# Optimization experiments

Hardware: AMD Instinct MI355X
Metric: run time of the kernel (lower is better)

## Reference

```python
import jax, jax.numpy as jnp
import numpy as np

PI = jnp.pi

def phasor_encode(x):
    # map phase in [-1,1] to unit complex phasor exp(i*pi*x)
    return jnp.exp(jnp.complex64(1j) * PI * x.astype(jnp.float32))

def phasor_act(z):
    # angle of complex activation, normalized back to [-1,1]
    return jnp.angle(z) / PI

def multi_dense(x, w, b):
    # PhasorMultiDense: x [b,t,d], w [h,d,D], b [h,D] (complex bias, ones init)
    xz = phasor_encode(x)                                      # [b,t,d] complex64
    wz = w.astype(jnp.complex64)
    bz = b.astype(jnp.complex64)
    yz = jnp.einsum('btd,hdD->bhtD', xz, wz) + bz[None, :, None, :]
    return phasor_act(yz)                                      # [b,h,t,D] real

def attend(q, k, v):
    # VSA phasor attention: similarity = Re(qz . conj(kz)) / d, softmax, complex bundle of v phasors
    d = q.shape[-1]
    qz = phasor_encode(q)
    kz = phasor_encode(k)
    scores = jnp.real(jnp.einsum('bhtd,bhTd->bhtT', qz, jnp.conj(kz))) / d
    probs = jax.nn.softmax(scores, axis=-1)
    vz = phasor_encode(v)
    out = jnp.einsum('bhtT,bhTd->bhtd', probs.astype(jnp.complex64), vz)
    return phasor_act(out)                                     # [b,h,t,D]

def setup_inputs() -> dict:
    key = jax.random.key(0)
    ks = jax.random.split(key, 8)
    B, Tq, Tkv, D, H = 2, 1024, 1024, 512, 8
    sw = 1.0 / np.sqrt(D)       # VarianceScaling(1.0) fan_in
    swo = 1.0 / np.sqrt(H * D)
    return {
        'query': jax.random.uniform(ks[0], (B, Tq, D), jnp.float32, -1.0, 1.0),
        'keyvalue': jax.random.uniform(ks[1], (B, Tkv, D), jnp.float32, -1.0, 1.0),
        'wq': jax.random.normal(ks[2], (H, D, D), jnp.float32) * sw,
        'bq': jnp.ones((H, D), jnp.float32),
        'wk': jax.random.normal(ks[3], (H, D, D), jnp.float32) * sw,
        'bk': jnp.ones((H, D), jnp.float32),
        'wv': jax.random.normal(ks[4], (H, D, D), jnp.float32) * sw,
        'bv': jnp.ones((H, D), jnp.float32),
        'wo': jax.random.normal(ks[5], (H * D, D), jnp.float32) * swo,
        'bo': jnp.ones((D,), jnp.float32),
    }

def reference(query, keyvalue, wq, bq, wk, bk, wv, bv, wo, bo):
    q = multi_dense(query, wq, bq)        # [b,h,t,D]
    k = multi_dense(keyvalue, wk, bk)
    v = multi_dense(keyvalue, wv, bv)
    r = attend(q, k, v)                   # [b,h,t,D]
    b_, h_, t_, d_ = r.shape
    r_flat = jnp.transpose(r, (0, 2, 1, 3)).reshape(b_, t_, h_ * d_)  # b t (h d)
    # final PhasorDense
    xz = phasor_encode(r_flat)
    z = jnp.einsum('btd,dD->btD', xz, wo.astype(jnp.complex64)) + bo.astype(jnp.complex64)
    return phasor_act(z)                  # [b, t_q, output_channels]
```

## Files before the change

kernel.cpp:

```cpp
#include <hip/hip_runtime.h>
#include <math.h>


#define PI_F 3.14159274101257324f

typedef __attribute__((ext_vector_type(8))) _Float16 half8;
typedef __attribute__((ext_vector_type(4))) _Float16 half4;
typedef __attribute__((ext_vector_type(2))) _Float16 half2v;
typedef __attribute__((ext_vector_type(4))) float f32x4;
typedef unsigned int u32;

#define MFMA16(a, b, c) __builtin_amdgcn_mfma_f32_16x16x32_f16((a), (b), (c), 0, 0, 0)

__device__ __forceinline__ void gll16(const void* g, void* l) {
    __builtin_amdgcn_global_load_lds(
        (const __attribute__((address_space(1))) u32*)g,
        (__attribute__((address_space(3))) u32*)l, 16, 0, 0);
}

#define MKSRC(U, NT, gh, gl, stride, sp, dp, dbase)                         \
    _Pragma("unroll") for (int u_ = 0; u_ < (U); ++u_) {                    \
        const int idx_ = u_ * (NT) + tid;                                   \
        const int row_ = idx_ >> 3, ss_ = idx_ & 7;                         \
        const int sl_ = ss_ ^ (row_ & 7);                                   \
        sp[u_] = ((sl_ < 4) ? (gh) : (gl)) + (size_t)row_ * (stride)        \
                 + (sl_ & 3) * 8;                                           \
        dp[u_] = (dbase) + idx_ * 16;                                       \
    }
#define STAGE(U, sp, dp, bufoff, kk)                                        \
    _Pragma("unroll") for (int u_ = 0; u_ < (U); ++u_)                      \
        gll16(sp[u_] + (kk), lds + (bufoff) + dp[u_]);

__device__ __forceinline__ half8 fragP(const char* ldsp, int row, int oct, int hilo) {
    const int sl = (oct + hilo * 4) ^ (row & 7);
    return *(const half8*)(ldsp + row * 128 + (sl << 4));
}

__device__ __forceinline__ void split2(float x, _Float16& h, _Float16& l) {
    _Float16 hh = (_Float16)x;
    h = hh;
    l = (_Float16)((x - (float)hh) * 4096.0f);
}

__global__ __launch_bounds__(256) void encode_phasor(
    const float* __restrict__ x,
    _Float16* __restrict__ ch, _Float16* __restrict__ cl,
    _Float16* __restrict__ sh, _Float16* __restrict__ sl)
{
    const int idx = blockIdx.x * 256 + threadIdx.x;
    float4 v = ((const float4*)x)[idx];
    float cc[4], ss[4];
    sincosf(PI_F * v.x, &ss[0], &cc[0]);
    sincosf(PI_F * v.y, &ss[1], &cc[1]);
    sincosf(PI_F * v.z, &ss[2], &cc[2]);
    sincosf(PI_F * v.w, &ss[3], &cc[3]);
    half4 chv, clv, shv, slv;
#pragma unroll
    for (int q = 0; q < 4; ++q) {
        _Float16 a, b;
        split2(cc[q], a, b); chv[q] = a; clv[q] = b;
        split2(ss[q], a, b); shv[q] = a; slv[q] = b;
    }
    ((half4*)ch)[idx] = chv;
    ((half4*)cl)[idx] = clv;
    ((half4*)sh)[idx] = shv;
    ((half4*)sl)[idx] = slv;
}

__global__ __launch_bounds__(256) void tsplit64(
    const float* __restrict__ w, _Float16* __restrict__ th, _Float16* __restrict__ tl,
    int K, int N)
{
    const int kt = blockIdx.x, ntile = blockIdx.y, h = blockIdx.z;
    const int k0 = kt * 64, n0 = ntile * 64;
    __shared__ float T[64][65];
    const int tid = threadIdx.x;
    const float* wb = w + (size_t)h * K * N;
    {
        const int r = tid >> 4, c4 = (tid & 15) * 4;
#pragma unroll
        for (int rr = 0; rr < 64; rr += 16) {
            float4 v = *(const float4*)&wb[(size_t)(k0 + rr + r) * N + n0 + c4];
            T[rr + r][c4 + 0] = v.x; T[rr + r][c4 + 1] = v.y;
            T[rr + r][c4 + 2] = v.z; T[rr + r][c4 + 3] = v.w;
        }
    }
    __syncthreads();
    {
        const int n = tid >> 2, kq = (tid & 3) * 16;
        half8 hv[2], lv[2];
#pragma unroll
        for (int q = 0; q < 16; ++q) {
            float f = T[kq + q][n];
            _Float16 hh, ll; split2(f, hh, ll);
            hv[q >> 3][q & 7] = hh; lv[q >> 3][q & 7] = ll;
        }
        _Float16* oh = th + ((size_t)h * N + n0 + n) * K + k0 + kq;
        _Float16* ol = tl + ((size_t)h * N + n0 + n) * K + k0 + kq;
        *(half8*)oh = hv[0]; *(half8*)(oh + 8) = hv[1];
        *(half8*)ol = lv[0]; *(half8*)(ol + 8) = lv[1];
    }
}

template<bool VT>
__global__ __launch_bounds__(256, 3) void proj_mfma(
    const _Float16* __restrict__ xch, const _Float16* __restrict__ xcl,
    const _Float16* __restrict__ xsh, const _Float16* __restrict__ xsl,
    const _Float16* __restrict__ wth, const _Float16* __restrict__ wtl,
    const float* __restrict__ bias,
    _Float16* __restrict__ o0h, _Float16* __restrict__ o0l,
    _Float16* __restrict__ vch, _Float16* __restrict__ vcl,
    _Float16* __restrict__ vsh, _Float16* __restrict__ vsl,
    int h0, int hcnt)
{
    const int m0 = blockIdx.x * 64;
    const int hc = blockIdx.y >> 3;
    const int n0 = (blockIdx.y & 7) * 64;
    __shared__ char lds[49152];
    const int tid = threadIdx.x, wv = tid >> 6, ln = tid & 63;
    const int wr = wv >> 1, wc = wv & 1, lm = ln & 15, oct = ln >> 4;

    const _Float16* sp_xc[2]; int dp_xc[2];
    const _Float16* sp_xs[2]; int dp_xs[2];
    const _Float16* sp_w[2];  int dp_w[2];
    MKSRC(2, 256, xch + (size_t)m0 * 512, xcl + (size_t)m0 * 512, 512, sp_xc, dp_xc, 0);
    MKSRC(2, 256, xsh + (size_t)m0 * 512, xsl + (size_t)m0 * 512, 512, sp_xs, dp_xs, 8192);
    const _Float16* wbh = wth + ((size_t)hc * 512 + n0) * 512;
    const _Float16* wbl = wtl + ((size_t)hc * 512 + n0) * 512;
    MKSRC(2, 256, wbh, wbl, 512, sp_w, dp_w, 16384);

    f32x4 ach[2][2] = {}, acl[2][2] = {}, ash[2][2] = {}, asl[2][2] = {};

    STAGE(2, sp_xc, dp_xc, 0, 0);
    STAGE(2, sp_xs, dp_xs, 0, 0);
    STAGE(2, sp_w,  dp_w,  0, 0);
    int off = 0;
    for (int s = 0; s < 16; ++s) {
        __syncthreads();
        const int nxt = off ^ 24576;
        if (s + 1 < 16) {
            const int kk = (s + 1) * 32;
            STAGE(2, sp_xc, dp_xc, nxt, kk);
            STAGE(2, sp_xs, dp_xs, nxt, kk);
            STAGE(2, sp_w,  dp_w,  nxt, kk);
        }
        const char* Xc = lds + off;
        const char* Xs = lds + off + 8192;
        const char* W  = lds + off + 16384;
        __builtin_amdgcn_s_setprio(1);
        half8 wh[2], wl[2];
#pragma unroll
        for (int j = 0; j < 2; ++j) {
            wh[j] = fragP(W, wc * 32 + j * 16 + lm, oct, 0);
            wl[j] = fragP(W, wc * 32 + j * 16 + lm, oct, 1);
        }
#pragma unroll
        for (int i = 0; i < 2; ++i) {
            const int ar = wr * 32 + i * 16 + lm;
            half8 c1 = fragP(Xc, ar, oct, 0);
            half8 c2 = fragP(Xc, ar, oct, 1);
            half8 s1 = fragP(Xs, ar, oct, 0);
            half8 s2 = fragP(Xs, ar, oct, 1);
#pragma unroll
            for (int j = 0; j < 2; ++j) {
                ach[i][j] = MFMA16(c1, wh[j], ach[i][j]);
                acl[i][j] = MFMA16(c1, wl[j], acl[i][j]);
                acl[i][j] = MFMA16(c2, wh[j], acl[i][j]);
                ash[i][j] = MFMA16(s1, wh[j], ash[i][j]);
                asl[i][j] = MFMA16(s1, wl[j], asl[i][j]);
                asl[i][j] = MFMA16(s2, wh[j], asl[i][j]);
            }
        }
        __builtin_amdgcn_s_setprio(0);
        off = nxt;
    }

    const float LS = 1.0f / 4096.0f;
    const int b = m0 >> 10, tbase = m0 & 1023;
    const size_t zz = (size_t)(b * hcnt + hc);
    if constexpr (!VT) {
#pragma unroll
        for (int j = 0; j < 2; ++j) {
            const int nloc = wc * 32 + j * 16 + lm;
            const float bval = bias[(size_t)(h0 + hc) * 512 + n0 + nloc];
#pragma unroll
            for (int i = 0; i < 2; ++i)
#pragma unroll
                for (int r = 0; r < 4; ++r) {
                    const int mloc = wr * 32 + i * 16 + oct * 4 + r;
                    float yc = ach[i][j][r] + acl[i][j][r] * LS + bval;
                    float ys = ash[i][j][r] + asl[i][j][r] * LS;
                    float inv = 1.0f / sqrtf(fmaxf(yc * yc + ys * ys, 1e-36f));
                    float c = yc * inv, sn = ys * inv;
                    _Float16 chh, chl, shh, shl;
                    split2(c, chh, chl); split2(sn, shh, shl);
                    const size_t offo = (zz * 1024 + tbase + mloc) * 1024 + 2 * (n0 + nloc);
                    half2v hv, lv;
                    hv[0] = chh; hv[1] = shh; lv[0] = chl; lv[1] = shl;
                    *(half2v*)(o0h + offo) = hv;
                    *(half2v*)(o0l + offo) = lv;
                }
        }
    } else {
#pragma unroll
        for (int q = 0; q < 2; ++q) {
            __syncthreads();
            if (wc == q) {
#pragma unroll
                for (int j = 0; j < 2; ++j) {
                    const int nloc = wc * 32 + j * 16 + lm;
                    const int dch = j * 16 + lm;
                    const float bval = bias[(size_t)(h0 + hc) * 512 + n0 + nloc];
#pragma unroll
                    for (int i = 0; i < 2; ++i)
#pragma unroll
                        for (int r = 0; r < 4; ++r) {
                            const int tloc = wr * 32 + i * 16 + oct * 4 + r;
                            float yc = ach[i][j][r] + acl[i][j][r] * LS + bval;
                            float ys = ash[i][j][r] + asl[i][j][r] * LS;
                            float inv = 1.0f / sqrtf(fmaxf(yc * yc + ys * ys, 1e-36f));
                            float c = yc * inv, sn = ys * inv;
                            _Float16 chh, chl, shh, shl;
                            split2(c, chh, chl); split2(sn, shh, shl);
                            ((_Float16*)(lds +     0))[dch * 68 + tloc] = chh;
                            ((_Float16*)(lds +  4352))[dch * 68 + tloc] = chl;
                            ((_Float16*)(lds +  8704))[dch * 68 + tloc] = shh;
                            ((_Float16*)(lds + 13056))[dch * 68 + tloc] = shl;
                        }
                }
            }
            __syncthreads();
            {
                const int p = tid >> 6, rem = tid & 63;
                const int dch = rem >> 1, seg = rem & 1;
                const _Float16* src = (const _Float16*)(lds + p * 4352) + dch * 68 + seg * 32;
                _Float16* outp = (p == 0) ? vch : (p == 1) ? vcl : (p == 2) ? vsh : vsl;
                _Float16* dst = outp + (zz * 512 + n0 + q * 32 + dch) * 1024 + tbase + seg * 32;
#pragma unroll
                for (int t = 0; t < 4; ++t)
                    *(half8*)(dst + t * 8) = *(const half8*)(src + t * 8);
            }
        }
    }
}

__global__ __launch_bounds__(256, 2) void scores_mfma(
    const _Float16* __restrict__ qzh, const _Float16* __restrict__ qzl,
    const _Float16* __restrict__ kzh, const _Float16* __restrict__ kzl,
    float* __restrict__ S)
{
    const int m0 = blockIdx.x * 128, n0 = blockIdx.y * 128, z = blockIdx.z;
    __shared__ char lds[65536];
    const size_t zb = (size_t)z << 20;
    const int tid = threadIdx.x, wv = tid >> 6, ln = tid & 63;
    const int wr = wv >> 1, wc = wv & 1, lm = ln & 15, oct = ln >> 4;

    const _Float16* sp_a[4]; int dp_a[4];
    const _Float16* sp_b[4]; int dp_b[4];
    MKSRC(4, 256, qzh + zb + (size_t)m0 * 1024, qzl + zb + (size_t)m0 * 1024, 1024, sp_a, dp_a, 0);
    MKSRC(4, 256, kzh + zb + (size_t)n0 * 1024, kzl + zb + (size_t)n0 * 1024, 1024, sp_b, dp_b, 16384);

    f32x4 acch[4][4] = {}, accl[4][4] = {};

    STAGE(4, sp_a, dp_a, 0, 0);
    STAGE(4, sp_b, dp_b, 0, 0);
    int off = 0;
    for (int s = 0; s < 32; ++s) {
        __syncthreads();
        const int nxt = off ^ 32768;
        if (s + 1 < 32) {
            const int kk = (s + 1) * 32;
            STAGE(4, sp_a, dp_a, nxt, kk);
            STAGE(4, sp_b, dp_b, nxt, kk);
        }
        const char* A = lds + off;
        const char* Bb = lds + off + 16384;
        __builtin_amdgcn_s_setprio(1);
        half8 bh[4], bl[4];
#pragma unroll
        for (int j = 0; j < 4; ++j) {
            bh[j] = fragP(Bb, wc * 64 + j * 16 + lm, oct, 0);
            bl[j] = fragP(Bb, wc * 64 + j * 16 + lm, oct, 1);
        }
#pragma unroll
        for (int i = 0; i < 4; ++i) {
            half8 ah = fragP(A, wr * 64 + i * 16 + lm, oct, 0);
            half8 al = fragP(A, wr * 64 + i * 16 + lm, oct, 1);
#pragma unroll
            for (int j = 0; j < 4; ++j) {
                acch[i][j] = MFMA16(ah, bh[j], acch[i][j]);
                accl[i][j] = MFMA16(ah, bl[j], accl[i][j]);
                accl[i][j] = MFMA16(al, bh[j], accl[i][j]);
            }
        }
        __builtin_amdgcn_s_setprio(0);
        off = nxt;
    }
    const float LS = 1.0f / 4096.0f, SC = 1.0f / 512.0f;
#pragma unroll
    for (int i = 0; i < 4; ++i)
#pragma unroll
        for (int j = 0; j < 4; ++j)
#pragma unroll
            for (int r = 0; r < 4; ++r) {
                const int row = m0 + wr * 64 + i * 16 + oct * 4 + r;
                const int col = n0 + wc * 64 + j * 16 + lm;
                S[zb + (size_t)row * 1024 + col] =
                    (acch[i][j][r] + accl[i][j][r] * LS) * SC;
            }
}

__global__ __launch_bounds__(256) void softmax_split(float* __restrict__ S)
{
    const size_t row = blockIdx.x;
    float* p = S + row * 1024;
    const int tid = threadIdx.x;
    float4 v = ((const float4*)p)[tid];
    float m = fmaxf(fmaxf(v.x, v.y), fmaxf(v.z, v.w));
#pragma unroll
    for (int off = 32; off >= 1; off >>= 1)
        m = fmaxf(m, __shfl_xor(m, off));
    __shared__ float redm[4], reds[4];
    const int wid = tid >> 6, lane = tid & 63;
    if (lane == 0) redm[wid] = m;
    __syncthreads();
    m = fmaxf(fmaxf(redm[0], redm[1]), fmaxf(redm[2], redm[3]));
    float4 e;
    e.x = expf(v.x - m); e.y = expf(v.y - m);
    e.z = expf(v.z - m); e.w = expf(v.w - m);
    float s = (e.x + e.y) + (e.z + e.w);
#pragma unroll
    for (int off = 32; off >= 1; off >>= 1)
        s += __shfl_xor(s, off);
    if (lane == 0) reds[wid] = s;
    __syncthreads();
    s = (reds[0] + reds[1]) + (reds[2] + reds[3]);
    e.x /= s; e.y /= s; e.z /= s; e.w /= s;
    __syncthreads();
    _Float16* ph = (_Float16*)p;
    half4 hv, lv;
    _Float16 a, b;
    split2(e.x, a, b); hv[0] = a; lv[0] = b;
    split2(e.y, a, b); hv[1] = a; lv[1] = b;
    split2(e.z, a, b); hv[2] = a; lv[2] = b;
    split2(e.w, a, b); hv[3] = a; lv[3] = b;
    *(half4*)(ph + tid * 4) = hv;
    *(half4*)(ph + 1024 + tid * 4) = lv;
}

__global__ __launch_bounds__(256, 2) void pv_mfma(
    const _Float16* __restrict__ P,
    const _Float16* __restrict__ vch, const _Float16* __restrict__ vcl,
    const _Float16* __restrict__ vsh, const _Float16* __restrict__ vsl,
    _Float16* __restrict__ rch, _Float16* __restrict__ rcl,
    _Float16* __restrict__ rsh, _Float16* __restrict__ rsl,
    int h0, int hcnt)
{
    const int m0 = blockIdx.x * 128, n0 = blockIdx.y * 64, z = blockIdx.z;
    __shared__ char lds[65536];
    const int tid = threadIdx.x, wv = tid >> 6, ln = tid & 63;
    const int wr = wv >> 1, wc = wv & 1, lm = ln & 15, oct = ln >> 4;

    const _Float16* Pb = P + (size_t)z * 1024 * 2048 + (size_t)m0 * 2048;
    const size_t vb = (size_t)z * 512 * 1024 + (size_t)n0 * 1024;
    const _Float16* sp_p[4];  int dp_p[4];
    const _Float16* sp_vc[2]; int dp_vc[2];
    const _Float16* sp_vs[2]; int dp_vs[2];
    MKSRC(4, 256, Pb, Pb + 1024, 2048, sp_p, dp_p, 0);
    MKSRC(2, 256, vch + vb, vcl + vb, 1024, sp_vc, dp_vc, 16384);
    MKSRC(2, 256, vsh + vb, vsl + vb, 1024, sp_vs, dp_vs, 24576);

    f32x4 ac_h[4][2] = {}, ac_l[4][2] = {}, as_h[4][2] = {}, as_l[4][2] = {};

    STAGE(4, sp_p,  dp_p,  0, 0);
    STAGE(2, sp_vc, dp_vc, 0, 0);
    STAGE(2, sp_vs, dp_vs, 0, 0);
    int off = 0;
    for (int s = 0; s < 32; ++s) {
        __syncthreads();
        const int nxt = off ^ 32768;
        if (s + 1 < 32) {
            const int kk = (s + 1) * 32;
            STAGE(4, sp_p,  dp_p,  nxt, kk);
            STAGE(2, sp_vc, dp_vc, nxt, kk);
            STAGE(2, sp_vs, dp_vs, nxt, kk);
        }
        const char* A  = lds + off;
        const char* Vc = lds + off + 16384;
        const char* Vs = lds + off + 24576;
        __builtin_amdgcn_s_setprio(1);
        half8 bc1[2], bc2[2], bs1[2], bs2[2];
#pragma unroll
        for (int j = 0; j < 2; ++j) {
            const int bn = wc * 32 + j * 16 + lm;
            bc1[j] = fragP(Vc, bn, oct, 0);
            bc2[j] = fragP(Vc, bn, oct, 1);
            bs1[j] = fragP(Vs, bn, oct, 0);
            bs2[j] = fragP(Vs, bn, oct, 1);
        }
#pragma unroll
        for (int i = 0; i < 4; ++i) {
            const int am = wr * 64 + i * 16 + lm;
            half8 ah = fragP(A, am, oct, 0);
            half8 al = fragP(A, am, oct, 1);
#pragma unroll
            for (int j = 0; j < 2; ++j) {
                ac_h[i][j] = MFMA16(ah, bc1[j], ac_h[i][j]);
                ac_l[i][j] = MFMA16(ah, bc2[j], ac_l[i][j]);
                ac_l[i][j] = MFMA16(al, bc1[j], ac_l[i][j]);
                as_h[i][j] = MFMA16(ah, bs1[j], as_h[i][j]);
                as_l[i][j] = MFMA16(ah, bs2[j], as_l[i][j]);
                as_l[i][j] = MFMA16(al, bs1[j], as_l[i][j]);
            }
        }
        __builtin_amdgcn_s_setprio(0);
        off = nxt;
    }
    const float LS = 1.0f / 4096.0f;
    const int b = z / hcnt, hg = h0 + z % hcnt;
#pragma unroll
    for (int i = 0; i < 4; ++i)
#pragma unroll
        for (int j = 0; j < 2; ++j)
#pragma unroll
            for (int r = 0; r < 4; ++r) {
                const int t = m0 + wr * 64 + i * 16 + oct * 4 + r;
                const int d = n0 + wc * 32 + j * 16 + lm;
                float zc = ac_h[i][j][r] + ac_l[i][j][r] * LS;
                float zs = as_h[i][j][r] + as_l[i][j][r] * LS;
                float inv = 1.0f / sqrtf(fmaxf(zc * zc + zs * zs, 1e-36f));
                float c = zc * inv, sn = zs * inv;
                _Float16 chh, chl, shh, shl;
                split2(c, chh, chl); split2(sn, shh, shl);
                const size_t offo = ((size_t)(b * 1024 + t)) * 4096 + (size_t)hg * 512 + d;
                rch[offo] = chh; rcl[offo] = chl; rsh[offo] = shh; rsl[offo] = shl;
            }
}

__global__ __launch_bounds__(256, 3) void final_mfma(
    const _Float16* __restrict__ rch, const _Float16* __restrict__ rcl,
    const _Float16* __restrict__ rsh, const _Float16* __restrict__ rsl,
    const _Float16* __restrict__ woh, const _Float16* __restrict__ wol,
    const float* __restrict__ bo, float* __restrict__ out)
{
    const int m0 = blockIdx.x * 64, n0 = blockIdx.y * 64;
    __shared__ char lds[49152];
    const int tid = threadIdx.x, wv = tid >> 6, ln = tid & 63;
    const int wr = wv >> 1, wc = wv & 1, lm = ln & 15, oct = ln >> 4;

    const _Float16* sp_rc[2]; int dp_rc[2];
    const _Float16* sp_rs[2]; int dp_rs[2];
    const _Float16* sp_w[2];  int dp_w[2];
    MKSRC(2, 256, rch + (size_t)m0 * 4096, rcl + (size_t)m0 * 4096, 4096, sp_rc, dp_rc, 0);
    MKSRC(2, 256, rsh + (size_t)m0 * 4096, rsl + (size_t)m0 * 4096, 4096, sp_rs, dp_rs, 8192);
    MKSRC(2, 256, woh + (size_t)n0 * 4096, wol + (size_t)n0 * 4096, 4096, sp_w, dp_w, 16384);

    f32x4 rr_h[2][2] = {}, rr_l[2][2] = {}, ri_h[2][2] = {}, ri_l[2][2] = {};

    STAGE(2, sp_rc, dp_rc, 0, 0);
    STAGE(2, sp_rs, dp_rs, 0, 0);
    STAGE(2, sp_w,  dp_w,  0, 0);
    int off = 0;
    for (int s = 0; s < 128; ++s) {
        __syncthreads();
        const int nxt = off ^ 24576;
        if (s + 1 < 128) {
            const int kk = (s + 1) * 32;
            STAGE(2, sp_rc, dp_rc, nxt, kk);
            STAGE(2, sp_rs, dp_rs, nxt, kk);
            STAGE(2, sp_w,  dp_w,  nxt, kk);
        }
        const char* Rc = lds + off;
        const char* Rs = lds + off + 8192;
        const char* W  = lds + off + 16384;
        __builtin_amdgcn_s_setprio(1);
        half8 wh[2], wl[2];
#pragma unroll
        for (int j = 0; j < 2; ++j) {
            wh[j] = fragP(W, wc * 32 + j * 16 + lm, oct, 0);
            wl[j] = fragP(W, wc * 32 + j * 16 + lm, oct, 1);
        }
#pragma unroll
        for (int i = 0; i < 2; ++i) {
            const int ar = wr * 32 + i * 16 + lm;
            half8 c1 = fragP(Rc, ar, oct, 0);
            half8 c2 = fragP(Rc, ar, oct, 1);
            half8 s1 = fragP(Rs, ar, oct, 0);
            half8 s2 = fragP(Rs, ar, oct, 1);
#pragma unroll
            for (int j = 0; j < 2; ++j) {
                rr_h[i][j] = MFMA16(c1, wh[j], rr_h[i][j]);
                rr_l[i][j] = MFMA16(c1, wl[j], rr_l[i][j]);
                rr_l[i][j] = MFMA16(c2, wh[j], rr_l[i][j]);
                ri_h[i][j] = MFMA16(s1, wh[j], ri_h[i][j]);
                ri_l[i][j] = MFMA16(s1, wl[j], ri_l[i][j]);
                ri_l[i][j] = MFMA16(s2, wh[j], ri_l[i][j]);
            }
        }
        __builtin_amdgcn_s_setprio(0);
        off = nxt;
    }
    const float LS = 1.0f / 4096.0f;
#pragma unroll
    for (int j = 0; j < 2; ++j) {
        const int nloc = wc * 32 + j * 16 + lm;
        const float bval = bo[n0 + nloc];
#pragma unroll
        for (int i = 0; i < 2; ++i)
#pragma unroll
            for (int r = 0; r < 4; ++r) {
                const int mloc = wr * 32 + i * 16 + oct * 4 + r;
                float zr = rr_h[i][j][r] + rr_l[i][j][r] * LS + bval;
                float zi = ri_h[i][j][r] + ri_l[i][j][r] * LS;
                out[(size_t)(m0 + mloc) * 512 + n0 + nloc] = atan2f(zi, zr) / PI_F;
            }
    }
}

extern "C" void kernel_launch(void* const* d_in, const int* in_sizes, int n_in,
                              void* d_out, int out_size, void* d_ws, size_t ws_size,
                              hipStream_t stream)
{
    (void)in_sizes; (void)n_in; (void)out_size;
    const float* query    = (const float*)d_in[0];
    const float* keyvalue = (const float*)d_in[1];
    const float* wq = (const float*)d_in[2];
    const float* bq = (const float*)d_in[3];
    const float* wk = (const float*)d_in[4];
    const float* bk = (const float*)d_in[5];
    const float* wv = (const float*)d_in[6];
    const float* bv = (const float*)d_in[7];
    const float* wo = (const float*)d_in[8];
    const float* bo = (const float*)d_in[9];
    float* out = (float*)d_out;

    int hcnt;
    if (ws_size >= (size_t)320 * 1024 * 1024) hcnt = 8;
    else if (ws_size >= (size_t)240 * 1024 * 1024) hcnt = 4;
    else hcnt = 2;
    const int Z = 2 * hcnt;

    char* p = (char*)d_ws;
    auto alloc = [&](size_t bytes) {
        char* r = p;
        p += (bytes + 255) & ~(size_t)255;
        return r;
    };
    const size_t PLX = (size_t)2048 * 512;
    _Float16* xq[4]; for (int i = 0; i < 4; ++i) xq[i] = (_Float16*)alloc(PLX * 2);
    _Float16* xk[4]; for (int i = 0; i < 4; ++i) xk[i] = (_Float16*)alloc(PLX * 2);
    _Float16* woT[2]; for (int i = 0; i < 2; ++i) woT[i] = (_Float16*)alloc((size_t)512 * 4096 * 2);
    const size_t WTE = (size_t)hcnt * 512 * 512;
    _Float16* wqT[2]; for (int i = 0; i < 2; ++i) wqT[i] = (_Float16*)alloc(WTE * 2);
    _Float16* wkT[2]; for (int i = 0; i < 2; ++i) wkT[i] = (_Float16*)alloc(WTE * 2);
    _Float16* wvT[2]; for (int i = 0; i < 2; ++i) wvT[i] = (_Float16*)alloc(WTE * 2);
    const size_t QZE = (size_t)Z * 1024 * 1024;
    _Float16* qz[2]; for (int i = 0; i < 2; ++i) qz[i] = (_Float16*)alloc(QZE * 2);
    _Float16* kz[2]; for (int i = 0; i < 2; ++i) kz[i] = (_Float16*)alloc(QZE * 2);
    float* S = (float*)alloc(QZE * 4);
    const size_t VTE = (size_t)Z * 512 * 1024;
    _Float16* vT[4]; for (int i = 0; i < 4; ++i) vT[i] = (_Float16*)alloc(VTE * 2);
    const size_t RCE = (size_t)2048 * 4096;
    _Float16* rcs[4];
    if (hcnt == 8) {
        for (int i = 0; i < 4; ++i) rcs[i] = (_Float16*)((char*)qz[0] + (size_t)i * RCE * 2);
    } else {
        for (int i = 0; i < 4; ++i) rcs[i] = (_Float16*)alloc(RCE * 2);
    }

    dim3 blk(256);

    encode_phasor<<<1024, blk, 0, stream>>>(query, xq[0], xq[1], xq[2], xq[3]);
    encode_phasor<<<1024, blk, 0, stream>>>(keyvalue, xk[0], xk[1], xk[2], xk[3]);
    tsplit64<<<dim3(64, 8, 1), blk, 0, stream>>>(wo, woT[0], woT[1], 4096, 512);

    for (int c = 0; c < 8 / hcnt; ++c) {
        const int h0 = c * hcnt;
        const float* wqc = wq + (size_t)h0 * 512 * 512;
        const float* wkc = wk + (size_t)h0 * 512 * 512;
        const float* wvc = wv + (size_t)h0 * 512 * 512;
        tsplit64<<<dim3(8, 8, hcnt), blk, 0, stream>>>(wqc, wqT[0], wqT[1], 512, 512);
        tsplit64<<<dim3(8, 8, hcnt), blk, 0, stream>>>(wkc, wkT[0], wkT[1], 512, 512);
        tsplit64<<<dim3(8, 8, hcnt), blk, 0, stream>>>(wvc, wvT[0], wvT[1], 512, 512);

        proj_mfma<false><<<dim3(32, 8 * hcnt), blk, 0, stream>>>(
            xq[0], xq[1], xq[2], xq[3], wqT[0], wqT[1], bq,
            qz[0], qz[1], nullptr, nullptr, nullptr, nullptr, h0, hcnt);
        proj_mfma<false><<<dim3(32, 8 * hcnt), blk, 0, stream>>>(
            xk[0], xk[1], xk[2], xk[3], wkT[0], wkT[1], bk,
            kz[0], kz[1], nullptr, nullptr, nullptr, nullptr, h0, hcnt);
        proj_mfma<true><<<dim3(32, 8 * hcnt), blk, 0, stream>>>(
            xk[0], xk[1], xk[2], xk[3], wvT[0], wvT[1], bv,
            nullptr, nullptr, vT[0], vT[1], vT[2], vT[3], h0, hcnt);

        scores_mfma<<<dim3(8, 8, Z), blk, 0, stream>>>(qz[0], qz[1], kz[0], kz[1], S);
        softmax_split<<<dim3(Z * 1024), blk, 0, stream>>>(S);
        pv_mfma<<<dim3(8, 8, Z), blk, 0, stream>>>(
            (const _Float16*)S, vT[0], vT[1], vT[2], vT[3],
            rcs[0], rcs[1], rcs[2], rcs[3], h0, hcnt);
    }

    final_mfma<<<dim3(32, 8), blk, 0, stream>>>(
        rcs[0], rcs[1], rcs[2], rcs[3], woT[0], woT[1], bo, out);
}
```

Measured before the change: 608.6 us.

## Move GEMMs to 32x32 MFMA, fuse Q/K projections, add XCD swizzle and split-K output

All GEMM kernels (projections, scores, PV and the final dense layer) switch from 16x16x32 to 32x32x16 MFMA, and the projection and final tiles widen to 128 columns with a larger LDS buffer. The Q and K projections become a single launch selected by blockIdx.z. The V projection gets a new two-round LDS transpose. The scores and PV kernels map their flattened grids with an XCD swizzle so neighbouring tiles land on the same XCD. The final dense layer is split along K into partial sums in a scratch buffer, reduced by a new combine kernel that adds the bias and takes atan2. This is meant to raise MFMA throughput, operand reuse and parallelism. The cost is more register pressure, an extra launch with partial-sum traffic, and split-K coverage that looks wrong for the smallest workspace setting.

```diff
diff --git a/kernel.cpp b/kernel.cpp
--- a/kernel.cpp
+++ b/kernel.cpp
@@ -7,10 +7,11 @@
 typedef __attribute__((ext_vector_type(8))) _Float16 half8;
 typedef __attribute__((ext_vector_type(4))) _Float16 half4;
 typedef __attribute__((ext_vector_type(2))) _Float16 half2v;
-typedef __attribute__((ext_vector_type(4))) float f32x4;
+typedef __attribute__((ext_vector_type(16))) float f32x16;
 typedef unsigned int u32;
 
-#define MFMA16(a, b, c) __builtin_amdgcn_mfma_f32_16x16x32_f16((a), (b), (c), 0, 0, 0)
+#define MFMA32(a, b, c) __builtin_amdgcn_mfma_f32_32x32x16_f16((a), (b), (c), 0, 0, 0)
+#define ROWOF(r, ln) (((r) & 3) + 8 * ((r) >> 2) + 4 * ((ln) >> 5))
 
 __device__ __forceinline__ void gll16(const void* g, void* l) {
     __builtin_amdgcn_global_load_lds(
@@ -42,6 +43,11 @@
     l = (_Float16)((x - (float)hh) * 4096.0f);
 }
 
+__device__ __forceinline__ int xcdswz(int bid, int nwg) {
+    const int cpx = nwg >> 3;
+    return (bid & 7) * cpx + (bid >> 3);
+}
+
 __global__ __launch_bounds__(256) void encode_phasor(
     const float* __restrict__ x,
     _Float16* __restrict__ ch, _Float16* __restrict__ cl,
@@ -102,74 +108,184 @@
     }
 }
 
-template<bool VT>
-__global__ __launch_bounds__(256, 3) void proj_mfma(
+__global__ __launch_bounds__(256, 2) void proj_qk(
+    const _Float16* __restrict__ qch, const _Float16* __restrict__ qcl,
+    const _Float16* __restrict__ qsh, const _Float16* __restrict__ qsl,
+    const _Float16* __restrict__ kch, const _Float16* __restrict__ kcl,
+    const _Float16* __restrict__ ksh, const _Float16* __restrict__ ksl,
+    const _Float16* __restrict__ wqh, const _Float16* __restrict__ wql,
+    const _Float16* __restrict__ wkh, const _Float16* __restrict__ wkl,
+    const float* __restrict__ bq, const float* __restrict__ bk,
+    _Float16* __restrict__ qzh, _Float16* __restrict__ qzl,
+    _Float16* __restrict__ kzh, _Float16* __restrict__ kzl,
+    int h0, int hcnt)
+{
+    const int inp = blockIdx.z;
+    const _Float16* xch = inp ? kch : qch;
+    const _Float16* xcl = inp ? kcl : qcl;
+    const _Float16* xsh = inp ? ksh : qsh;
+    const _Float16* xsl = inp ? ksl : qsl;
+    const _Float16* wth = inp ? wkh : wqh;
+    const _Float16* wtl = inp ? wkl : wql;
+    const float* bias = inp ? bk : bq;
+    _Float16* ozh = inp ? kzh : qzh;
+    _Float16* ozl = inp ? kzl : qzl;
+
+    const int m0 = blockIdx.x * 64;
+    const int hc = blockIdx.y >> 2;
+    const int n0 = (blockIdx.y & 3) * 128;
+    __shared__ char lds[65536];
+    const int tid = threadIdx.x, wv = tid >> 6, ln = tid & 63;
+    const int wr = wv >> 1, wc = wv & 1, lm32 = ln & 31, lh = ln >> 5;
+
+    const _Float16* sp_xc[2]; int dp_xc[2];
+    const _Float16* sp_xs[2]; int dp_xs[2];
+    const _Float16* sp_w[4];  int dp_w[4];
+    MKSRC(2, 256, xch + (size_t)m0 * 512, xcl + (size_t)m0 * 512, 512, sp_xc, dp_xc, 0);
+    MKSRC(2, 256, xsh + (size_t)m0 * 512, xsl + (size_t)m0 * 512, 512, sp_xs, dp_xs, 8192);
+    const _Float16* wbh = wth + ((size_t)hc * 512 + n0) * 512;
+    const _Float16* wbl = wtl + ((size_t)hc * 512 + n0) * 512;
+    MKSRC(4, 256, wbh, wbl, 512, sp_w, dp_w, 16384);
+
+    f32x16 ach[2] = {}, acl[2] = {}, ash[2] = {}, asl[2] = {};
+
+    STAGE(2, sp_xc, dp_xc, 0, 0);
+    STAGE(2, sp_xs, dp_xs, 0, 0);
+    STAGE(4, sp_w,  dp_w,  0, 0);
+    int off = 0;
+    for (int s = 0; s < 16; ++s) {
+        __syncthreads();
+        const int nxt = off ^ 32768;
+        if (s + 1 < 16) {
+            const int kk = (s + 1) * 32;
+            STAGE(2, sp_xc, dp_xc, nxt, kk);
+            STAGE(2, sp_xs, dp_xs, nxt, kk);
+            STAGE(4, sp_w,  dp_w,  nxt, kk);
+        }
+        const char* Xc = lds + off;
+        const char* Xs = lds + off + 8192;
+        const char* W  = lds + off + 16384;
+        __builtin_amdgcn_s_setprio(1);
+#pragma unroll
+        for (int kw = 0; kw < 2; ++kw) {
+            const int oct = kw * 2 + lh;
+            half8 wh0 = fragP(W, wc * 64 + lm32, oct, 0);
+            half8 wh1 = fragP(W, wc * 64 + 32 + lm32, oct, 0);
+            half8 wl0 = fragP(W, wc * 64 + lm32, oct, 1);
+            half8 wl1 = fragP(W, wc * 64 + 32 + lm32, oct, 1);
+            half8 c1 = fragP(Xc, wr * 32 + lm32, oct, 0);
+            half8 c2 = fragP(Xc, wr * 32 + lm32, oct, 1);
+            half8 s1 = fragP(Xs, wr * 32 + lm32, oct, 0);
+            half8 s2 = fragP(Xs, wr * 32 + lm32, oct, 1);
+            ach[0] = MFMA32(c1, wh0, ach[0]);
+            acl[0] = MFMA32(c1, wl0, acl[0]);
+            acl[0] = MFMA32(c2, wh0, acl[0]);
+            ash[0] = MFMA32(s1, wh0, ash[0]);
+            asl[0] = MFMA32(s1, wl0, asl[0]);
+            asl[0] = MFMA32(s2, wh0, asl[0]);
+            ach[1] = MFMA32(c1, wh1, ach[1]);
+            acl[1] = MFMA32(c1, wl1, acl[1]);
+            acl[1] = MFMA32(c2, wh1, acl[1]);
+            ash[1] = MFMA32(s1, wh1, ash[1]);
+            asl[1] = MFMA32(s1, wl1, asl[1]);
+            asl[1] = MFMA32(s2, wh1, asl[1]);
+        }
+        __builtin_amdgcn_s_setprio(0);
+        off = nxt;
+    }
+
+    const float LS = 1.0f / 4096.0f;
+    const int b = m0 >> 10, tbase = m0 & 1023;
+    const size_t zz = (size_t)(b * hcnt + hc);
+#pragma unroll
+    for (int j = 0; j < 2; ++j) {
+        const int nloc = wc * 64 + j * 32 + lm32;
+        const float bval = bias[(size_t)(h0 + hc) * 512 + n0 + nloc];
+#pragma unroll
+        for (int r = 0; r < 16; ++r) {
+            const int mloc = wr * 32 + ROWOF(r, ln);
+            float yc = ach[j][r] + acl[j][r] * LS + bval;
+            float ys = ash[j][r] + asl[j][r] * LS;
+            float inv = 1.0f / sqrtf(fmaxf(yc * yc + ys * ys, 1e-36f));
+            float c = yc * inv, sn = ys * inv;
+            _Float16 chh, chl, shh, shl;
+            split2(c, chh, chl); split2(sn, shh, shl);
+            const size_t offo = (zz * 1024 + tbase + mloc) * 1024 + 2 * (n0 + nloc);
+            half2v hv, lv;
+            hv[0] = chh; hv[1] = shh; lv[0] = chl; lv[1] = shl;
+            *(half2v*)(ozh + offo) = hv;
+            *(half2v*)(ozl + offo) = lv;
+        }
+    }
+}
+
+__global__ __launch_bounds__(256, 2) void proj_v(
     const _Float16* __restrict__ xch, const _Float16* __restrict__ xcl,
     const _Float16* __restrict__ xsh, const _Float16* __restrict__ xsl,
     const _Float16* __restrict__ wth, const _Float16* __restrict__ wtl,
     const float* __restrict__ bias,
-    _Float16* __restrict__ o0h, _Float16* __restrict__ o0l,
     _Float16* __restrict__ vch, _Float16* __restrict__ vcl,
     _Float16* __restrict__ vsh, _Float16* __restrict__ vsl,
     int h0, int hcnt)
 {
     const int m0 = blockIdx.x * 64;
-    const int hc = blockIdx.y >> 3;
-    const int n0 = (blockIdx.y & 7) * 64;
-    __shared__ char lds[49152];
+    const int hc = blockIdx.y >> 2;
+    const int n0 = (blockIdx.y & 3) * 128;
+    __shared__ char lds[65536];
     const int tid = threadIdx.x, wv = tid >> 6, ln = tid & 63;
-    const int wr = wv >> 1, wc = wv & 1, lm = ln & 15, oct = ln >> 4;
+    const int wr = wv >> 1, wc = wv & 1, lm32 = ln & 31, lh = ln >> 5;
 
     const _Float16* sp_xc[2]; int dp_xc[2];
     const _Float16* sp_xs[2]; int dp_xs[2];
-    const _Float16* sp_w[2];  int dp_w[2];
+    const _Float16* sp_w[4];  int dp_w[4];
     MKSRC(2, 256, xch + (size_t)m0 * 512, xcl + (size_t)m0 * 512, 512, sp_xc, dp_xc, 0);
     MKSRC(2, 256, xsh + (size_t)m0 * 512, xsl + (size_t)m0 * 512, 512, sp_xs, dp_xs, 8192);
     const _Float16* wbh = wth + ((size_t)hc * 512 + n0) * 512;
     const _Float16* wbl = wtl + ((size_t)hc * 512 + n0) * 512;
-    MKSRC(2, 256, wbh, wbl, 512, sp_w, dp_w, 16384);
-
-    f32x4 ach[2][2] = {}, acl[2][2] = {}, ash[2][2] = {}, asl[2][2] = {};
+    MKSRC(4, 256, wbh, wbl, 512, sp_w, dp_w, 16384);
+
+    f32x16 ach[2] = {}, acl[2] = {}, ash[2] = {}, asl[2] = {};
 
     STAGE(2, sp_xc, dp_xc, 0, 0);
     STAGE(2, sp_xs, dp_xs, 0, 0);
-    STAGE(2, sp_w,  dp_w,  0, 0);
+    STAGE(4, sp_w,  dp_w,  0, 0);
     int off = 0;
     for (int s = 0; s < 16; ++s) {
         __syncthreads();
-        const int nxt = off ^ 24576;
+        const int nxt = off ^ 32768;
         if (s + 1 < 16) {
             const int kk = (s + 1) * 32;
             STAGE(2, sp_xc, dp_xc, nxt, kk);
             STAGE(2, sp_xs, dp_xs, nxt, kk);
-            STAGE(2, sp_w,  dp_w,  nxt, kk);
+            STAGE(4, sp_w,  dp_w,  nxt, kk);
         }
         const char* Xc = lds + off;
         const char* Xs = lds + off + 8192;
         const char* W  = lds + off + 16384;
         __builtin_amdgcn_s_setprio(1);
-        half8 wh[2], wl[2];
-#pragma unroll
-        for (int j = 0; j < 2; ++j) {
-            wh[j] = fragP(W, wc * 32 + j * 16 + lm, oct, 0);
-            wl[j] = fragP(W, wc * 32 + j * 16 + lm, oct, 1);
-        }
-#pragma unroll
-        for (int i = 0; i < 2; ++i) {
-            const int ar = wr * 32 + i * 16 + lm;
-            half8 c1 = fragP(Xc, ar, oct, 0);
-            half8 c2 = fragP(Xc, ar, oct, 1);
-            half8 s1 = fragP(Xs, ar, oct, 0);
-            half8 s2 = fragP(Xs, ar, oct, 1);
-#pragma unroll
-            for (int j = 0; j < 2; ++j) {
-                ach[i][j] = MFMA16(c1, wh[j], ach[i][j]);
-                acl[i][j] = MFMA16(c1, wl[j], acl[i][j]);
-                acl[i][j] = MFMA16(c2, wh[j], acl[i][j]);
-                ash[i][j] = MFMA16(s1, wh[j], ash[i][j]);
-                asl[i][j] = MFMA16(s1, wl[j], asl[i][j]);
-                asl[i][j] = MFMA16(s2, wh[j], asl[i][j]);
-            }
+#pragma unroll
+        for (int kw = 0; kw < 2; ++kw) {
+            const int oct = kw * 2 + lh;
+            half8 wh0 = fragP(W, wc * 64 + lm32, oct, 0);
+            half8 wh1 = fragP(W, wc * 64 + 32 + lm32, oct, 0);
+            half8 wl0 = fragP(W, wc * 64 + lm32, oct, 1);
+            half8 wl1 = fragP(W, wc * 64 + 32 + lm32, oct, 1);
+            half8 c1 = fragP(Xc, wr * 32 + lm32, oct, 0);
+            half8 c2 = fragP(Xc, wr * 32 + lm32, oct, 1);
+            half8 s1 = fragP(Xs, wr * 32 + lm32, oct, 0);
+            half8 s2 = fragP(Xs, wr * 32 + lm32, oct, 1);
+            ach[0] = MFMA32(c1, wh0, ach[0]);
+            acl[0] = MFMA32(c1, wl0, acl[0]);
+            acl[0] = MFMA32(c2, wh0, acl[0]);
+            ash[0] = MFMA32(s1, wh0, ash[0]);
+            asl[0] = MFMA32(s1, wl0, asl[0]);
+            asl[0] = MFMA32(s2, wh0, asl[0]);
+            ach[1] = MFMA32(c1, wh1, ach[1]);
+            acl[1] = MFMA32(c1, wl1, acl[1]);
+            acl[1] = MFMA32(c2, wh1, acl[1]);
+            ash[1] = MFMA32(s1, wh1, ash[1]);
+            asl[1] = MFMA32(s1, wl1, asl[1]);
+            asl[1] = MFMA32(s2, wh1, asl[1]);
         }
         __builtin_amdgcn_s_setprio(0);
         off = nxt;
@@ -178,68 +294,36 @@
     const float LS = 1.0f / 4096.0f;
     const int b = m0 >> 10, tbase = m0 & 1023;
     const size_t zz = (size_t)(b * hcnt + hc);
-    if constexpr (!VT) {
+    _Float16* T = (_Float16*)lds;
+#pragma unroll
+    for (int round = 0; round < 2; ++round) {
+        __syncthreads();
 #pragma unroll
         for (int j = 0; j < 2; ++j) {
-            const int nloc = wc * 32 + j * 16 + lm;
-            const float bval = bias[(size_t)(h0 + hc) * 512 + n0 + nloc];
-#pragma unroll
-            for (int i = 0; i < 2; ++i)
-#pragma unroll
-                for (int r = 0; r < 4; ++r) {
-                    const int mloc = wr * 32 + i * 16 + oct * 4 + r;
-                    float yc = ach[i][j][r] + acl[i][j][r] * LS + bval;
-                    float ys = ash[i][j][r] + asl[i][j][r] * LS;
-                    float inv = 1.0f / sqrtf(fmaxf(yc * yc + ys * ys, 1e-36f));
-                    float c = yc * inv, sn = ys * inv;
-                    _Float16 chh, chl, shh, shl;
-                    split2(c, chh, chl); split2(sn, shh, shl);
-                    const size_t offo = (zz * 1024 + tbase + mloc) * 1024 + 2 * (n0 + nloc);
-                    half2v hv, lv;
-                    hv[0] = chh; hv[1] = shh; lv[0] = chl; lv[1] = shl;
-                    *(half2v*)(o0h + offo) = hv;
-                    *(half2v*)(o0l + offo) = lv;
-                }
-        }
-    } else {
-#pragma unroll
-        for (int q = 0; q < 2; ++q) {
-            __syncthreads();
-            if (wc == q) {
-#pragma unroll
-                for (int j = 0; j < 2; ++j) {
-                    const int nloc = wc * 32 + j * 16 + lm;
-                    const int dch = j * 16 + lm;
-                    const float bval = bias[(size_t)(h0 + hc) * 512 + n0 + nloc];
-#pragma unroll
-                    for (int i = 0; i < 2; ++i)
-#pragma unroll
-                        for (int r = 0; r < 4; ++r) {
-                            const int tloc = wr * 32 + i * 16 + oct * 4 + r;
-                            float yc = ach[i][j][r] + acl[i][j][r] * LS + bval;
-                            float ys = ash[i][j][r] + asl[i][j][r] * LS;
-                            float inv = 1.0f / sqrtf(fmaxf(yc * yc + ys * ys, 1e-36f));
-                            float c = yc * inv, sn = ys * inv;
-                            _Float16 chh, chl, shh, shl;
-                            split2(c, chh, chl); split2(sn, shh, shl);
-                            ((_Float16*)(lds +     0))[dch * 68 + tloc] = chh;
-                            ((_Float16*)(lds +  4352))[dch * 68 + tloc] = chl;
-                            ((_Float16*)(lds +  8704))[dch * 68 + tloc] = shh;
-                            ((_Float16*)(lds + 13056))[dch * 68 + tloc] = shl;
-                        }
-                }
+            const int dloc = wc * 64 + j * 32 + lm32;
+            const float bval = bias[(size_t)(h0 + hc) * 512 + n0 + dloc];
+#pragma unroll
+            for (int r = 0; r < 16; ++r) {
+                const int tloc = wr * 32 + ROWOF(r, ln);
+                float yc = ach[j][r] + acl[j][r] * LS + bval;
+                float ys = ash[j][r] + asl[j][r] * LS;
+                float inv = 1.0f / sqrtf(fmaxf(yc * yc + ys * ys, 1e-36f));
+                float val = (round ? ys : yc) * inv;
+                _Float16 hh, ll;
+                split2(val, hh, ll);
+                T[dloc * 72 + tloc] = hh;
+                T[9216 + dloc * 72 + tloc] = ll;
             }
-            __syncthreads();
-            {
-                const int p = tid >> 6, rem = tid & 63;
-                const int dch = rem >> 1, seg = rem & 1;
-                const _Float16* src = (const _Float16*)(lds + p * 4352) + dch * 68 + seg * 32;
-                _Float16* outp = (p == 0) ? vch : (p == 1) ? vcl : (p == 2) ? vsh : vsl;
-                _Float16* dst = outp + (zz * 512 + n0 + q * 32 + dch) * 1024 + tbase + seg * 32;
-#pragma unroll
-                for (int t = 0; t < 4; ++t)
-                    *(half8*)(dst + t * 8) = *(const half8*)(src + t * 8);
-            }
+        }
+        __syncthreads();
+        {
+            const int p2 = tid >> 7, d = tid & 127;
+            const _Float16* src = T + p2 * 9216 + d * 72;
+            _Float16* plane = (round == 0) ? (p2 ? vcl : vch) : (p2 ? vsl : vsh);
+            _Float16* dst = plane + (zz * 512 + n0 + d) * 1024 + tbase;
+#pragma unroll
+            for (int q = 0; q < 8; ++q)
+                *(half8*)(dst + q * 8) = *(const half8*)(src + q * 8);
         }
     }
 }
@@ -247,20 +331,23 @@
 __global__ __launch_bounds__(256, 2) void scores_mfma(
     const _Float16* __restrict__ qzh, const _Float16* __restrict__ qzl,
     const _Float16* __restrict__ kzh, const _Float16* __restrict__ kzl,
-    float* __restrict__ S)
-{
-    const int m0 = blockIdx.x * 128, n0 = blockIdx.y * 128, z = blockIdx.z;
+    float* __restrict__ S, int Z)
+{
+    const int wg = xcdswz(blockIdx.x, Z * 64);
+    const int z = wg >> 6;
+    const int rem = wg & 63;
+    const int m0 = (rem & 7) << 7, n0 = (rem >> 3) << 7;
     __shared__ char lds[65536];
     const size_t zb = (size_t)z << 20;
     const int tid = threadIdx.x, wv = tid >> 6, ln = tid & 63;
-    const int wr = wv >> 1, wc = wv & 1, lm = ln & 15, oct = ln >> 4;
+    const int wr = wv >> 1, wc = wv & 1, lm32 = ln & 31, lh = ln >> 5;
 
     const _Float16* sp_a[4]; int dp_a[4];
     const _Float16* sp_b[4]; int dp_b[4];
     MKSRC(4, 256, qzh + zb + (size_t)m0 * 1024, qzl + zb + (size_t)m0 * 1024, 1024, sp_a, dp_a, 0);
     MKSRC(4, 256, kzh + zb + (size_t)n0 * 1024, kzl + zb + (size_t)n0 * 1024, 1024, sp_b, dp_b, 16384);
 
-    f32x4 acch[4][4] = {}, accl[4][4] = {};
+    f32x16 acch[2][2] = {}, accl[2][2] = {};
 
     STAGE(4, sp_a, dp_a, 0, 0);
     STAGE(4, sp_b, dp_b, 0, 0);
@@ -273,24 +360,26 @@
             STAGE(4, sp_a, dp_a, nxt, kk);
             STAGE(4, sp_b, dp_b, nxt, kk);
         }
-        const char* A = lds + off;
+        const char* A  = lds + off;
         const char* Bb = lds + off + 16384;
         __builtin_amdgcn_s_setprio(1);
-        half8 bh[4], bl[4];
-#pragma unroll
-        for (int j = 0; j < 4; ++j) {
-            bh[j] = fragP(Bb, wc * 64 + j * 16 + lm, oct, 0);
-            bl[j] = fragP(Bb, wc * 64 + j * 16 + lm, oct, 1);
-        }
-#pragma unroll
-        for (int i = 0; i < 4; ++i) {
-            half8 ah = fragP(A, wr * 64 + i * 16 + lm, oct, 0);
-            half8 al = fragP(A, wr * 64 + i * 16 + lm, oct, 1);
-#pragma unroll
-            for (int j = 0; j < 4; ++j) {
-                acch[i][j] = MFMA16(ah, bh[j], acch[i][j]);
-                accl[i][j] = MFMA16(ah, bl[j], accl[i][j]);
-                accl[i][j] = MFMA16(al, bh[j], accl[i][j]);
+#pragma unroll
+        for (int kw = 0; kw < 2; ++kw) {
+            const int oct = kw * 2 + lh;
+            half8 bh0 = fragP(Bb, wc * 64 + lm32, oct, 0);
+            half8 bh1 = fragP(Bb, wc * 64 + 32 + lm32, oct, 0);
+            half8 bl0 = fragP(Bb, wc * 64 + lm32, oct, 1);
+            half8 bl1 = fragP(Bb, wc * 64 + 32 + lm32, oct, 1);
+#pragma unroll
+            for (int i = 0; i < 2; ++i) {
+                half8 qh = fragP(A, wr * 64 + i * 32 + lm32, oct, 0);
+                half8 ql = fragP(A, wr * 64 + i * 32 + lm32, oct, 1);
+                acch[i][0] = MFMA32(qh, bh0, acch[i][0]);
+                accl[i][0] = MFMA32(qh, bl0, accl[i][0]);
+                accl[i][0] = MFMA32(ql, bh0, accl[i][0]);
+                acch[i][1] = MFMA32(qh, bh1, acch[i][1]);
+                accl[i][1] = MFMA32(qh, bl1, accl[i][1]);
+                accl[i][1] = MFMA32(ql, bh1, accl[i][1]);
             }
         }
         __builtin_amdgcn_s_setprio(0);
@@ -298,13 +387,13 @@
     }
     const float LS = 1.0f / 4096.0f, SC = 1.0f / 512.0f;
 #pragma unroll
-    for (int i = 0; i < 4; ++i)
-#pragma unroll
-        for (int j = 0; j < 4; ++j)
-#pragma unroll
-            for (int r = 0; r < 4; ++r) {
-                const int row = m0 + wr * 64 + i * 16 + oct * 4 + r;
-                const int col = n0 + wc * 64 + j * 16 + lm;
+    for (int i = 0; i < 2; ++i)
+#pragma unroll
+        for (int j = 0; j < 2; ++j)
+#pragma unroll
+            for (int r = 0; r < 16; ++r) {
+                const int row = m0 + wr * 64 + i * 32 + ROWOF(r, ln);
+                const int col = n0 + wc * 64 + j * 32 + lm32;
                 S[zb + (size_t)row * 1024 + col] =
                     (acch[i][j][r] + accl[i][j][r] * LS) * SC;
             }
@@ -354,12 +443,15 @@
     const _Float16* __restrict__ vsh, const _Float16* __restrict__ vsl,
     _Float16* __restrict__ rch, _Float16* __restrict__ rcl,
     _Float16* __restrict__ rsh, _Float16* __restrict__ rsl,
-    int h0, int hcnt)
-{
-    const int m0 = blockIdx.x * 128, n0 = blockIdx.y * 64, z = blockIdx.z;
+    int h0, int hcnt, int Z)
+{
+    const int wg = xcdswz(blockIdx.x, Z * 64);
+    const int z = wg >> 6;
+    const int rem = wg & 63;
+    const int m0 = (rem & 7) << 7, n0 = (rem >> 3) << 6;
     __shared__ char lds[65536];
     const int tid = threadIdx.x, wv = tid >> 6, ln = tid & 63;
-    const int wr = wv >> 1, wc = wv & 1, lm = ln & 15, oct = ln >> 4;
+    const int wr = wv >> 1, wc = wv & 1, lm32 = ln & 31, lh = ln >> 5;
 
     const _Float16* Pb = P + (size_t)z * 1024 * 2048 + (size_t)m0 * 2048;
     const size_t vb = (size_t)z * 512 * 1024 + (size_t)n0 * 1024;
@@ -370,7 +462,7 @@
     MKSRC(2, 256, vch + vb, vcl + vb, 1024, sp_vc, dp_vc, 16384);
     MKSRC(2, 256, vsh + vb, vsl + vb, 1024, sp_vs, dp_vs, 24576);
 
-    f32x4 ac_h[4][2] = {}, ac_l[4][2] = {}, as_h[4][2] = {}, as_l[4][2] = {};
+    f32x16 ac_h[2] = {}, ac_l[2] = {}, as_h[2] = {}, as_l[2] = {};
 
     STAGE(4, sp_p,  dp_p,  0, 0);
     STAGE(2, sp_vc, dp_vc, 0, 0);
@@ -389,28 +481,23 @@
         const char* Vc = lds + off + 16384;
         const char* Vs = lds + off + 24576;
         __builtin_amdgcn_s_setprio(1);
-        half8 bc1[2], bc2[2], bs1[2], bs2[2];
-#pragma unroll
-        for (int j = 0; j < 2; ++j) {
-            const int bn = wc * 32 + j * 16 + lm;
-            bc1[j] = fragP(Vc, bn, oct, 0);
-            bc2[j] = fragP(Vc, bn, oct, 1);
-            bs1[j] = fragP(Vs, bn, oct, 0);
-            bs2[j] = fragP(Vs, bn, oct, 1);
-        }
-#pragma unroll
-        for (int i = 0; i < 4; ++i) {
-            const int am = wr * 64 + i * 16 + lm;
-            half8 ah = fragP(A, am, oct, 0);
-            half8 al = fragP(A, am, oct, 1);
-#pragma unroll
-            for (int j = 0; j < 2; ++j) {
-                ac_h[i][j] = MFMA16(ah, bc1[j], ac_h[i][j]);
-                ac_l[i][j] = MFMA16(ah, bc2[j], ac_l[i][j]);
-                ac_l[i][j] = MFMA16(al, bc1[j], ac_l[i][j]);
-                as_h[i][j] = MFMA16(ah, bs1[j], as_h[i][j]);
-                as_l[i][j] = MFMA16(ah, bs2[j], as_l[i][j]);
-                as_l[i][j] = MFMA16(al, bs1[j], as_l[i][j]);
+#pragma unroll
+        for (int kw = 0; kw < 2; ++kw) {
+            const int oct = kw * 2 + lh;
+            half8 vc1 = fragP(Vc, wc * 32 + lm32, oct, 0);
+            half8 vc2 = fragP(Vc, wc * 32 + lm32, oct, 1);
+            half8 vs1 = fragP(Vs, wc * 32 + lm32, oct, 0);
+            half8 vs2 = fragP(Vs, wc * 32 + lm32, oct, 1);
+#pragma unroll
+            for (int i = 0; i < 2; ++i) {
+                half8 ph = fragP(A, wr * 64 + i * 32 + lm32, oct, 0);
+                half8 pl = fragP(A, wr * 64 + i * 32 + lm32, oct, 1);
+                ac_h[i] = MFMA32(ph, vc1, ac_h[i]);
+                ac_l[i] = MFMA32(ph, vc2, ac_l[i]);
+                ac_l[i] = MFMA32(pl, vc1, ac_l[i]);
+                as_h[i] = MFMA32(ph, vs1, as_h[i]);
+                as_l[i] = MFMA32(ph, vs2, as_l[i]);
+                as_l[i] = MFMA32(pl, vs1, as_l[i]);
             }
         }
         __builtin_amdgcn_s_setprio(0);
@@ -419,83 +506,84 @@
     const float LS = 1.0f / 4096.0f;
     const int b = z / hcnt, hg = h0 + z % hcnt;
 #pragma unroll
-    for (int i = 0; i < 4; ++i)
-#pragma unroll
-        for (int j = 0; j < 2; ++j)
-#pragma unroll
-            for (int r = 0; r < 4; ++r) {
-                const int t = m0 + wr * 64 + i * 16 + oct * 4 + r;
-                const int d = n0 + wc * 32 + j * 16 + lm;
-                float zc = ac_h[i][j][r] + ac_l[i][j][r] * LS;
-                float zs = as_h[i][j][r] + as_l[i][j][r] * LS;
-                float inv = 1.0f / sqrtf(fmaxf(zc * zc + zs * zs, 1e-36f));
-                float c = zc * inv, sn = zs * inv;
-                _Float16 chh, chl, shh, shl;
-                split2(c, chh, chl); split2(sn, shh, shl);
-                const size_t offo = ((size_t)(b * 1024 + t)) * 4096 + (size_t)hg * 512 + d;
-                rch[offo] = chh; rcl[offo] = chl; rsh[offo] = shh; rsl[offo] = shl;
-            }
-}
-
-__global__ __launch_bounds__(256, 3) void final_mfma(
+    for (int i = 0; i < 2; ++i)
+#pragma unroll
+        for (int r = 0; r < 16; ++r) {
+            const int t = m0 + wr * 64 + i * 32 + ROWOF(r, ln);
+            const int d = n0 + wc * 32 + lm32;
+            float zc = ac_h[i][r] + ac_l[i][r] * LS;
+            float zs = as_h[i][r] + as_l[i][r] * LS;
+            float inv = 1.0f / sqrtf(fmaxf(zc * zc + zs * zs, 1e-36f));
+            float c = zc * inv, sn = zs * inv;
+            _Float16 chh, chl, shh, shl;
+            split2(c, chh, chl); split2(sn, shh, shl);
+            const size_t offo = ((size_t)(b * 1024 + t)) * 4096 + (size_t)hg * 512 + d;
+            rch[offo] = chh; rcl[offo] = chl; rsh[offo] = shh; rsl[offo] = shl;
+        }
+}
+
+__global__ __launch_bounds__(256, 2) void final_mfma(
     const _Float16* __restrict__ rch, const _Float16* __restrict__ rcl,
     const _Float16* __restrict__ rsh, const _Float16* __restrict__ rsl,
     const _Float16* __restrict__ woh, const _Float16* __restrict__ wol,
-    const float* __restrict__ bo, float* __restrict__ out)
-{
-    const int m0 = blockIdx.x * 64, n0 = blockIdx.y * 64;
-    __shared__ char lds[49152];
+    float* __restrict__ pbuf)
+{
+    const int m0 = blockIdx.x * 64, n0 = blockIdx.y * 128;
+    const int ks = blockIdx.z;
+    const size_t kbase = (size_t)ks * 1024;
+    __shared__ char lds[65536];
     const int tid = threadIdx.x, wv = tid >> 6, ln = tid & 63;
-    const int wr = wv >> 1, wc = wv & 1, lm = ln & 15, oct = ln >> 4;
+    const int wr = wv >> 1, wc = wv & 1, lm32 = ln & 31, lh = ln >> 5;
 
     const _Float16* sp_rc[2]; int dp_rc[2];
     const _Float16* sp_rs[2]; int dp_rs[2];
-    const _Float16* sp_w[2];  int dp_w[2];
-    MKSRC(2, 256, rch + (size_t)m0 * 4096, rcl + (size_t)m0 * 4096, 4096, sp_rc, dp_rc, 0);
-    MKSRC(2, 256, rsh + (size_t)m0 * 4096, rsl + (size_t)m0 * 4096, 4096, sp_rs, dp_rs, 8192);
-    MKSRC(2, 256, woh + (size_t)n0 * 4096, wol + (size_t)n0 * 4096, 4096, sp_w, dp_w, 16384);
-
-    f32x4 rr_h[2][2] = {}, rr_l[2][2] = {}, ri_h[2][2] = {}, ri_l[2][2] = {};
+    const _Float16* sp_w[4];  int dp_w[4];
+    MKSRC(2, 256, rch + (size_t)m0 * 4096 + kbase, rcl + (size_t)m0 * 4096 + kbase, 4096, sp_rc, dp_rc, 0);
+    MKSRC(2, 256, rsh + (size_t)m0 * 4096 + kbase, rsl + (size_t)m0 * 4096 + kbase, 4096, sp_rs, dp_rs, 8192);
+    MKSRC(4, 256, woh + (size_t)n0 * 4096 + kbase, wol + (size_t)n0 * 4096 + kbase, 4096, sp_w, dp_w, 16384);
+
+    f32x16 rr_h[2] = {}, rr_l[2] = {}, ri_h[2] = {}, ri_l[2] = {};
 
     STAGE(2, sp_rc, dp_rc, 0, 0);
     STAGE(2, sp_rs, dp_rs, 0, 0);
-    STAGE(2, sp_w,  dp_w,  0, 0);
+    STAGE(4, sp_w,  dp_w,  0, 0);
     int off = 0;
-    for (int s = 0; s < 128; ++s) {
+    for (int s = 0; s < 32; ++s) {
         __syncthreads();
-        const int nxt = off ^ 24576;
-        if (s + 1 < 128) {
+        const int nxt = off ^ 32768;
+        if (s + 1 < 32) {
             const int kk = (s + 1) * 32;
             STAGE(2, sp_rc, dp_rc, nxt, kk);
             STAGE(2, sp_rs, dp_rs, nxt, kk);
-            STAGE(2, sp_w,  dp_w,  nxt, kk);
+            STAGE(4, sp_w,  dp_w,  nxt, kk);
         }
         const char* Rc = lds + off;
         const char* Rs = lds + off + 8192;
         const char* W  = lds + off + 16384;
         __builtin_amdgcn_s_setprio(1);
-        half8 wh[2], wl[2];
-#pragma unroll
-        for (int j = 0; j < 2; ++j) {
-            wh[j] = fragP(W, wc * 32 + j * 16 + lm, oct, 0);
-            wl[j] = fragP(W, wc * 32 + j * 16 + lm, oct, 1);
-        }
-#pragma unroll
-        for (int i = 0; i < 2; ++i) {
-            const int ar = wr * 32 + i * 16 + lm;
-            half8 c1 = fragP(Rc, ar, oct, 0);
-            half8 c2 = fragP(Rc, ar, oct, 1);
-            half8 s1 = fragP(Rs, ar, oct, 0);
-            half8 s2 = fragP(Rs, ar, oct, 1);
-#pragma unroll
-            for (int j = 0; j < 2; ++j) {
-                rr_h[i][j] = MFMA16(c1, wh[j], rr_h[i][j]);
-                rr_l[i][j] = MFMA16(c1, wl[j], rr_l[i][j]);
-                rr_l[i][j] = MFMA16(c2, wh[j], rr_l[i][j]);
-                ri_h[i][j] = MFMA16(s1, wh[j], ri_h[i][j]);
-                ri_l[i][j] = MFMA16(s1, wl[j], ri_l[i][j]);
-                ri_l[i][j] = MFMA16(s2, wh[j], ri_l[i][j]);
-            }
+#pragma unroll
+        for (int kw = 0; kw < 2; ++kw) {
+            const int oct = kw * 2 + lh;
+            half8 wh0 = fragP(W, wc * 64 + lm32, oct, 0);
+            half8 wh1 = fragP(W, wc * 64 + 32 + lm32, oct, 0);
+            half8 wl0 = fragP(W, wc * 64 + lm32, oct, 1);
+            half8 wl1 = fragP(W, wc * 64 + 32 + lm32, oct, 1);
+            half8 c1 = fragP(Rc, wr * 32 + lm32, oct, 0);
+            half8 c2 = fragP(Rc, wr * 32 + lm32, oct, 1);
+            half8 s1 = fragP(Rs, wr * 32 + lm32, oct, 0);
+            half8 s2 = fragP(Rs, wr * 32 + lm32, oct, 1);
+            rr_h[0] = MFMA32(c1, wh0, rr_h[0]);
+            rr_l[0] = MFMA32(c1, wl0, rr_l[0]);
+            rr_l[0] = MFMA32(c2, wh0, rr_l[0]);
+            ri_h[0] = MFMA32(s1, wh0, ri_h[0]);
+            ri_l[0] = MFMA32(s1, wl0, ri_l[0]);
+            ri_l[0] = MFMA32(s2, wh0, ri_l[0]);
+            rr_h[1] = MFMA32(c1, wh1, rr_h[1]);
+            rr_l[1] = MFMA32(c1, wl1, rr_l[1]);
+            rr_l[1] = MFMA32(c2, wh1, rr_l[1]);
+            ri_h[1] = MFMA32(s1, wh1, ri_h[1]);
+            ri_l[1] = MFMA32(s1, wl1, ri_l[1]);
+            ri_l[1] = MFMA32(s2, wh1, ri_l[1]);
         }
         __builtin_amdgcn_s_setprio(0);
         off = nxt;
@@ -503,18 +591,31 @@
     const float LS = 1.0f / 4096.0f;
 #pragma unroll
     for (int j = 0; j < 2; ++j) {
-        const int nloc = wc * 32 + j * 16 + lm;
-        const float bval = bo[n0 + nloc];
-#pragma unroll
-        for (int i = 0; i < 2; ++i)
-#pragma unroll
-            for (int r = 0; r < 4; ++r) {
-                const int mloc = wr * 32 + i * 16 + oct * 4 + r;
-                float zr = rr_h[i][j][r] + rr_l[i][j][r] * LS + bval;
-                float zi = ri_h[i][j][r] + ri_l[i][j][r] * LS;
-                out[(size_t)(m0 + mloc) * 512 + n0 + nloc] = atan2f(zi, zr) / PI_F;
-            }
-    }
+        const int ng = n0 + wc * 64 + j * 32 + lm32;
+#pragma unroll
+        for (int r = 0; r < 16; ++r) {
+            const int mg = m0 + wr * 32 + ROWOF(r, ln);
+            float zr = rr_h[j][r] + rr_l[j][r] * LS;
+            float zi = ri_h[j][r] + ri_l[j][r] * LS;
+            float2 v; v.x = zr; v.y = zi;
+            *(float2*)&pbuf[((size_t)(ks * 2048 + mg) * 512 + ng) * 2] = v;
+        }
+    }
+}
+
+__global__ __launch_bounds__(256) void final_combine(
+    const float* __restrict__ pbuf, const float* __restrict__ bo,
+    float* __restrict__ out, int KS)
+{
+    const int m = blockIdx.x, t = threadIdx.x;
+    float4 acc = {0.f, 0.f, 0.f, 0.f};
+    for (int s = 0; s < KS; ++s) {
+        float4 v = *(const float4*)&pbuf[(size_t)(s * 2048 + m) * 1024 + t * 4];
+        acc.x += v.x; acc.y += v.y; acc.z += v.z; acc.w += v.w;
+    }
+    const int n0 = t * 2;
+    out[(size_t)m * 512 + n0]     = atan2f(acc.y, acc.x + bo[n0]) / PI_F;
+    out[(size_t)m * 512 + n0 + 1] = atan2f(acc.w, acc.z + bo[n0 + 1]) / PI_F;
 }
 
 extern "C" void kernel_launch(void* const* d_in, const int* in_sizes, int n_in,
@@ -539,6 +640,7 @@
     else if (ws_size >= (size_t)240 * 1024 * 1024) hcnt = 4;
     else hcnt = 2;
     const int Z = 2 * hcnt;
+    const int KS = (hcnt == 2) ? 2 : 4;
 
     char* p = (char*)d_ws;
     auto alloc = [&](size_t bytes) {
@@ -567,6 +669,7 @@
     } else {
         for (int i = 0; i < 4; ++i) rcs[i] = (_Float16*)alloc(RCE * 2);
     }
+    float* pbuf = (float*)kz[0];
 
     dim3 blk(256);
 
@@ -583,23 +686,22 @@
         tsplit64<<<dim3(8, 8, hcnt), blk, 0, stream>>>(wkc, wkT[0], wkT[1], 512, 512);
         tsplit64<<<dim3(8, 8, hcnt), blk, 0, stream>>>(wvc, wvT[0], wvT[1], 512, 512);
 
-        proj_mfma<false><<<dim3(32, 8 * hcnt), blk, 0, stream>>>(
-            xq[0], xq[1], xq[2], xq[3], wqT[0], wqT[1], bq,
-            qz[0], qz[1], nullptr, nullptr, nullptr, nullptr, h0, hcnt);
-        proj_mfma<false><<<dim3(32, 8 * hcnt), blk, 0, stream>>>(
-            xk[0], xk[1], xk[2], xk[3], wkT[0], wkT[1], bk,
-            kz[0], kz[1], nullptr, nullptr, nullptr, nullptr, h0, hcnt);
-        proj_mfma<true><<<dim3(32, 8 * hcnt), blk, 0, stream>>>(
+        proj_qk<<<dim3(32, 4 * hcnt, 2), blk, 0, stream>>>(
+            xq[0], xq[1], xq[2], xq[3], xk[0], xk[1], xk[2], xk[3],
+            wqT[0], wqT[1], wkT[0], wkT[1], bq, bk,
+            qz[0], qz[1], kz[0], kz[1], h0, hcnt);
+        proj_v<<<dim3(32, 4 * hcnt), blk, 0, stream>>>(
             xk[0], xk[1], xk[2], xk[3], wvT[0], wvT[1], bv,
-            nullptr, nullptr, vT[0], vT[1], vT[2], vT[3], h0, hcnt);
-
-        scores_mfma<<<dim3(8, 8, Z), blk, 0, stream>>>(qz[0], qz[1], kz[0], kz[1], S);
+            vT[0], vT[1], vT[2], vT[3], h0, hcnt);
+
+        scores_mfma<<<dim3(Z * 64), blk, 0, stream>>>(qz[0], qz[1], kz[0], kz[1], S, Z);
         softmax_split<<<dim3(Z * 1024), blk, 0, stream>>>(S);
-        pv_mfma<<<dim3(8, 8, Z), blk, 0, stream>>>(
+        pv_mfma<<<dim3(Z * 64), blk, 0, stream>>>(
             (const _Float16*)S, vT[0], vT[1], vT[2], vT[3],
-            rcs[0], rcs[1], rcs[2], rcs[3], h0, hcnt);
-    }
-
-    final_mfma<<<dim3(32, 8), blk, 0, stream>>>(
-        rcs[0], rcs[1], rcs[2], rcs[3], woT[0], woT[1], bo, out);
-}
+            rcs[0], rcs[1], rcs[2], rcs[3], h0, hcnt, Z);
+    }
+
+    final_mfma<<<dim3(32, 4, KS), blk, 0, stream>>>(
+        rcs[0], rcs[1], rcs[2], rcs[3], woT[0], woT[1], pbuf);
+    final_combine<<<dim3(2048), blk, 0, stream>>>(pbuf, bo, out, KS);
+}
```

After: 579.9 us. -4.7%, faster.
